# Kernel optimization log

Hardware: AMD Instinct MI355X
Metric: run time of the kernel (lower is better)

Reference implementation:

```python
import jax, jax.numpy as jnp
import numpy as np

BITS = 8
NUM_HEADS = 16
EMB = 1024
MLP = 4096
BATCH = 4
SEQ = 1024


def _fq(x, bits, signed=True, narrow=False):
    """Fake-quantize with per-tensor absmax scale (brevitas MinMax/MaxStats style),
    straight-through-estimator round. signed+narrow => weight quant; signed non-narrow
    => activation quant; unsigned => QuantReLU output."""
    if signed:
        qmax = 2.0 ** (bits - 1) - 1.0
        qmin = -qmax if narrow else -(qmax + 1.0)
    else:
        qmax = 2.0 ** bits - 1.0
        qmin = 0.0
    scale = jax.lax.stop_gradient(jnp.max(jnp.abs(x)) / qmax)
    scale = jnp.maximum(scale, jnp.asarray(1e-8, x.dtype))
    q = x / scale
    q = q + jax.lax.stop_gradient(jnp.round(q) - q)  # STE round
    return jnp.clip(q, qmin, qmax) * scale


def _layernorm(x, eps=1e-5):
    mu = jnp.mean(x, axis=-1, keepdims=True)
    var = jnp.mean(jnp.square(x - mu), axis=-1, keepdims=True)
    return (x - mu) * jax.lax.rsqrt(var + eps)


def setup_inputs() -> dict:
    key = jax.random.key(0)
    ks = jax.random.split(key, 11)
    def w(k, shape, fan_in):
        return jax.random.normal(k, shape, jnp.float32) * (1.0 / np.sqrt(fan_in))
    return {
        "x": jax.random.normal(ks[0], (BATCH, SEQ, EMB), jnp.float32),
        "Wq": w(ks[1], (EMB, EMB), EMB), "bq": jnp.zeros((EMB,), jnp.float32),
        "Wk": w(ks[2], (EMB, EMB), EMB), "bk": jnp.zeros((EMB,), jnp.float32),
        "Wv": w(ks[3], (EMB, EMB), EMB), "bv": jnp.zeros((EMB,), jnp.float32),
        "Wo": w(ks[4], (EMB, EMB), EMB), "bo": jnp.zeros((EMB,), jnp.float32),
        "W1": w(ks[5], (MLP, EMB), EMB), "b1": jnp.zeros((MLP,), jnp.float32),
        "W2": w(ks[6], (EMB, MLP), MLP), "b2": jnp.zeros((EMB,), jnp.float32),
    }


def reference(x, Wq, bq, Wk, bk, Wv, bv, Wo, bo, W1, b1, W2, b2):
    B, S, E = x.shape
    H, D = NUM_HEADS, EMB // NUM_HEADS
    fqw = lambda W: _fq(W, BITS, signed=True, narrow=True)   # weight quant
    fqb = lambda b: _fq(b, BITS, signed=True)                # bias quant
    fqa = lambda a: _fq(a, BITS, signed=True)                # act quant

    # sdp_input_quant
    qx = fqa(x)
    # separate (unpacked) in-projections, torch Linear: y = x @ W.T + b
    q = qx @ fqw(Wq).T + fqb(bq)
    k = qx @ fqw(Wk).T + fqb(bk)
    v = qx @ fqw(Wv).T + fqb(bv)
    # [B,H,S,D]
    q = q.reshape(B, S, H, D).transpose(0, 2, 1, 3)
    k = k.reshape(B, S, H, D).transpose(0, 2, 1, 3)
    v = v.reshape(B, S, H, D).transpose(0, 2, 1, 3)

    q_scaled = fqa(q * (1.0 / np.sqrt(D)))          # q_scaled_quant
    k_t = fqa(k.transpose(0, 1, 3, 2))              # k_transposed_quant
    v = fqa(v)                                      # v_quant

    scores = jnp.einsum('bhqd,bhdk->bhqk', q_scaled, k_t)
    scores = fqa(scores)                            # softmax_input_quant
    attn = jax.nn.softmax(scores, axis=-1)
    attn = fqa(attn)                                # attn_output_weights_quant

    ctx = jnp.einsum('bhqk,bhkd->bhqd', attn, v)
    ctx = ctx.transpose(0, 2, 1, 3).reshape(B, S, E)
    ctx = fqa(ctx)                                  # out_proj_input_quant
    attn_out = ctx @ fqw(Wo).T + fqb(bo)

    # residual_sdp (QuantEltwiseAdd input quant on both operands) + layer-norm
    h = _layernorm(fqa(x) + fqa(attn_out))

    # MLP: QuantIdentity -> QuantLinear -> QuantReLU(unsigned) -> QuantLinear
    m = fqa(h)
    m = m @ fqw(W1).T + fqb(b1)
    m = _fq(jax.nn.relu(m), BITS, signed=False)
    m = m @ fqw(W2).T + fqb(b2)

    return _layernorm(fqa(h) + fqa(m))
```

## Files before the change

kernel.cpp:

```cpp
#include <hip/hip_runtime.h>
#include <cstdint>
#include <cstddef>

#define TB_B 4
#define TB_S 1024
#define TB_E 1024
#define TB_H 16
#define TB_D 64
#define TB_MLP 4096
#define TB_ROWS (TB_B * TB_S)

typedef int int4v __attribute__((ext_vector_type(4)));

#define LGKM0() __asm__ volatile("s_waitcnt lgkmcnt(0)" ::: "memory")
#define CMEMBAR() __asm__ volatile("" ::: "memory")

static __device__ __forceinline__ void atomicMaxF(float* addr, float v) {
  atomicMax(reinterpret_cast<unsigned int*>(addr), __float_as_uint(v));
}

static __device__ __forceinline__ float fast_exp2(float x) {
#if __has_builtin(__builtin_amdgcn_exp2f)
  return __builtin_amdgcn_exp2f(x);
#else
  return exp2f(x);
#endif
}

static __device__ __forceinline__ void gl2lds16(const void* g, void* l) {
  __builtin_amdgcn_global_load_lds(
      (const __attribute__((address_space(1))) void*)g,
      (__attribute__((address_space(3))) void*)l, 16, 0, 0);
}

struct AMDesc { const float* p; long n4; int slot; };
struct AMBatch { AMDesc d[13]; };
__global__ __launch_bounds__(256) void absmax_multi_kernel(AMBatch bt, float* ws) {
  AMDesc d = bt.d[blockIdx.y];
  float m = 0.f;
  long stride = (long)gridDim.x * 256;
  for (long i = (long)blockIdx.x * 256 + threadIdx.x; i < d.n4; i += stride) {
    float4 v = ((const float4*)d.p)[i];
    m = fmaxf(m, fmaxf(fmaxf(fabsf(v.x), fabsf(v.y)), fmaxf(fabsf(v.z), fabsf(v.w))));
  }
#pragma unroll
  for (int o = 32; o; o >>= 1) m = fmaxf(m, __shfl_down(m, o, 64));
  __shared__ float sm[4];
  if (!(threadIdx.x & 63)) sm[threadIdx.x >> 6] = m;
  __syncthreads();
  if (threadIdx.x == 0)
    atomicMaxF(ws + d.slot, fmaxf(fmaxf(sm[0], sm[1]), fmaxf(sm[2], sm[3])));
}

struct QMDesc { const float* in; signed char* out; long n4; int slot; float qmin; };
struct QMBatch { QMDesc d[7]; };
__global__ __launch_bounds__(256) void quant8_multi_kernel(QMBatch bt, const float* ws) {
  QMDesc d = bt.d[blockIdx.y];
  float scale = fmaxf(ws[d.slot] / 127.f, 1e-8f);
  long stride = (long)gridDim.x * 256;
  for (long i = (long)blockIdx.x * 256 + threadIdx.x; i < d.n4; i += stride) {
    float4 v = ((const float4*)d.in)[i];
    char4 o;
    o.x = (signed char)(int)fminf(fmaxf(rintf(v.x / scale), d.qmin), 127.f);
    o.y = (signed char)(int)fminf(fmaxf(rintf(v.y / scale), d.qmin), 127.f);
    o.z = (signed char)(int)fminf(fmaxf(rintf(v.z / scale), d.qmin), 127.f);
    o.w = (signed char)(int)fminf(fmaxf(rintf(v.w / scale), d.qmin), 127.f);
    ((char4*)d.out)[i] = o;
  }
}

struct BDesc { const float* in; float* out; int n4; int slot; };
struct BBatch { BDesc d[6]; };
__global__ __launch_bounds__(256) void bias_quant_multi_kernel(BBatch bt, const float* ws) {
  BDesc d = bt.d[blockIdx.y];
  float scale = fmaxf(ws[d.slot] / 127.f, 1e-8f);
  int i = blockIdx.x * 256 + threadIdx.x;
  if (i < d.n4) {
    float4 v = ((const float4*)d.in)[i];
    float4 o;
    o.x = fminf(fmaxf(rintf(v.x / scale), -128.f), 127.f) * scale;
    o.y = fminf(fmaxf(rintf(v.y / scale), -128.f), 127.f) * scale;
    o.z = fminf(fmaxf(rintf(v.z / scale), -128.f), 127.f) * scale;
    o.w = fminf(fmaxf(rintf(v.w / scale), -128.f), 127.f) * scale;
    ((float4*)d.out)[i] = o;
  }
}

__global__ __launch_bounds__(256) void quant8_kernel(const float* __restrict__ in,
                                                     signed char* __restrict__ out8, long n4,
                                                     const float* __restrict__ amax_p,
                                                     float pre, float qmin) {
  float scale = fmaxf(amax_p[0] * pre / 127.f, 1e-8f);
  long stride = (long)gridDim.x * 256;
  for (long i = (long)blockIdx.x * 256 + threadIdx.x; i < n4; i += stride) {
    float4 v = ((const float4*)in)[i];
    char4 o;
    o.x = (signed char)(int)fminf(fmaxf(rintf(v.x * pre / scale), qmin), 127.f);
    o.y = (signed char)(int)fminf(fmaxf(rintf(v.y * pre / scale), qmin), 127.f);
    o.z = (signed char)(int)fminf(fmaxf(rintf(v.z * pre / scale), qmin), 127.f);
    o.w = (signed char)(int)fminf(fmaxf(rintf(v.w * pre / scale), qmin), 127.f);
    ((char4*)out8)[i] = o;
  }
}

__global__ __launch_bounds__(256) void relu_quant8_kernel(const float* __restrict__ in,
                                                          signed char* __restrict__ out8, long n4,
                                                          const float* __restrict__ amax_p) {
  float scale = fmaxf(amax_p[0] / 255.f, 1e-8f);
  long stride = (long)gridDim.x * 256;
  for (long i = (long)blockIdx.x * 256 + threadIdx.x; i < n4; i += stride) {
    float4 v = ((const float4*)in)[i];
    char4 o;
    o.x = (signed char)((int)fminf(fmaxf(rintf(fmaxf(v.x, 0.f) / scale), 0.f), 255.f) - 128);
    o.y = (signed char)((int)fminf(fmaxf(rintf(fmaxf(v.y, 0.f) / scale), 0.f), 255.f) - 128);
    o.z = (signed char)((int)fminf(fmaxf(rintf(fmaxf(v.z, 0.f) / scale), 0.f), 255.f) - 128);
    o.w = (signed char)((int)fminf(fmaxf(rintf(fmaxf(v.w, 0.f) / scale), 0.f), 255.f) - 128);
    ((char4*)out8)[i] = o;
  }
}

__global__ __launch_bounds__(256) void rowsum_i8_kernel(const signed char* __restrict__ w8,
                                                        int* __restrict__ out, int Kdim) {
  const int row = blockIdx.x, t = threadIdx.x;
  const signed char* p = w8 + (long)row * Kdim;
  int s = 0;
  for (int i = t * 16; i < Kdim; i += 4096) {
    int4v v = *(const int4v*)(p + i);
    const signed char* b = (const signed char*)&v;
#pragma unroll
    for (int j = 0; j < 16; j++) s += b[j];
  }
#pragma unroll
  for (int o = 32; o; o >>= 1) s += __shfl_down(s, o, 64);
  __shared__ int sm[4];
  if (!(t & 63)) sm[t >> 6] = s;
  __syncthreads();
  if (t == 0) out[row] = sm[0] + sm[1] + sm[2] + sm[3];
}

__global__ __launch_bounds__(256) void gemm_i8_kernel(
    const signed char* __restrict__ A, const signed char* __restrict__ Bw,
    const float* __restrict__ biasq,
    const float* __restrict__ amax_a, float div_a,
    const float* __restrict__ amax_b,
    const int* __restrict__ rowsum,
    float* __restrict__ C, int M, int N, int K,
    float* __restrict__ amax_out, int relu_amax, int mode) {
  __shared__ signed char As[8192];
  __shared__ signed char Bs[8192];
  const int t = threadIdx.x;
  int bx, by;
  {
    int lin = blockIdx.y * gridDim.x + blockIdx.x;
    if ((gridDim.y & 7) == 0) {
      int xcd = lin & 7, j = lin >> 3;
      bx = j % gridDim.x;
      by = (gridDim.y >> 3) * xcd + j / gridDim.x;
    } else { bx = blockIdx.x; by = blockIdx.y; }
  }
  const int m0 = by * 128, n0 = bx * 128;
  const int w = t >> 6, lane = t & 63;
  const int fr = lane & 15, quad = lane >> 4;
  const int r0 = t >> 2;
  const int c0 = (t & 3) * 16;
  const int a_off0 = (w * 32 + fr) * 64 + quad * 16;
  const int b_off0 = fr * 64 + quad * 16;

  int4v acc[2][8];
#pragma unroll
  for (int r = 0; r < 2; r++)
#pragma unroll
    for (int c = 0; c < 8; c++) acc[r][c] = (int4v){0, 0, 0, 0};

  for (int k0 = 0; k0 < K; k0 += 64) {
    __syncthreads();
    gl2lds16(A + (long)(m0 + r0) * K + k0 + c0, As + t * 16);
    gl2lds16(A + (long)(m0 + r0 + 64) * K + k0 + c0, As + t * 16 + 4096);
    gl2lds16(Bw + (long)(n0 + r0) * K + k0 + c0, Bs + t * 16);
    gl2lds16(Bw + (long)(n0 + r0 + 64) * K + k0 + c0, Bs + t * 16 + 4096);
    __syncthreads();
    int4v af[2], bf[8];
#pragma unroll
    for (int r = 0; r < 2; r++) af[r] = *(const int4v*)(As + a_off0 + r * 1024);
#pragma unroll
    for (int c = 0; c < 8; c++) bf[c] = *(const int4v*)(Bs + b_off0 + c * 1024);
#pragma unroll
    for (int r = 0; r < 2; r++)
#pragma unroll
      for (int c = 0; c < 8; c++)
        acc[r][c] = __builtin_amdgcn_mfma_i32_16x16x64_i8(af[r], bf[c], acc[r][c], 0, 0, 0);
  }

  const int seg = (mode == 1) ? (n0 >> 10) : 0;
  const float s_a = fmaxf(amax_a[0] / div_a, 1e-8f);
  const float s_b = fmaxf(amax_b[seg] / 127.f, 1e-8f);
  const float s = s_a * s_b;
  float lmax = 0.f;
#pragma unroll
  for (int r = 0; r < 2; r++) {
    int rbase = m0 + w * 32 + r * 16 + quad * 4;
#pragma unroll
    for (int c = 0; c < 8; c++) {
      int col = n0 + c * 16 + fr;
      int corr = rowsum ? (rowsum[col] << 7) : 0;
      float bi = biasq[col];
      if (mode == 1) {
        int h = (col >> 6) & 15, dd = col & 63;
        float* cbase = C + (long)seg * ((long)TB_ROWS * TB_E);
#pragma unroll
        for (int g = 0; g < 4; g++) {
          int m = rbase + g;
          int b = m >> 10, sdx = m & 1023;
          float o = (float)acc[r][c][g] * s + bi;
          lmax = fmaxf(lmax, fabsf(o));
          cbase[((((long)b * TB_H + h) * TB_S) + sdx) * TB_D + dd] = o;
        }
      } else {
#pragma unroll
        for (int g = 0; g < 4; g++) {
          float o = (float)(acc[r][c][g] + corr) * s + bi;
          lmax = fmaxf(lmax, relu_amax ? fmaxf(o, 0.f) : fabsf(o));
          C[(long)(rbase + g) * N + col] = o;
        }
      }
    }
  }
#pragma unroll
  for (int o = 32; o; o >>= 1) lmax = fmaxf(lmax, __shfl_down(lmax, o, 64));
  __shared__ float redm[4];
  if (!lane) redm[w] = lmax;
  __syncthreads();
  if (t == 0) atomicMaxF(amax_out + seg, fmaxf(fmaxf(redm[0], redm[1]), fmaxf(redm[2], redm[3])));
}

__global__ __launch_bounds__(256) void quant8_vb_kernel(const float* __restrict__ v,
                                                        const float* __restrict__ amax_p,
                                                        signed char* __restrict__ v8b) {
  __shared__ signed char tile[64][80];
  const int bh = blockIdx.x;
  const int jb = blockIdx.y;
  const int s0 = jb * 64;
  const int t = threadIdx.x;
  const float scale = fmaxf(amax_p[0] / 127.f, 1e-8f);
#pragma unroll
  for (int it = 0; it < 4; it++) {
    int idx = t + it * 256;
    int r = idx >> 4, c4 = (idx & 15) * 4;
    float4 vv = *(const float4*)(v + ((long)bh * TB_S + s0 + r) * TB_D + c4);
    tile[c4 + 0][r] = (signed char)(int)fminf(fmaxf(rintf(vv.x / scale), -128.f), 127.f);
    tile[c4 + 1][r] = (signed char)(int)fminf(fmaxf(rintf(vv.y / scale), -128.f), 127.f);
    tile[c4 + 2][r] = (signed char)(int)fminf(fmaxf(rintf(vv.z / scale), -128.f), 127.f);
    tile[c4 + 3][r] = (signed char)(int)fminf(fmaxf(rintf(vv.w / scale), -128.f), 127.f);
  }
  __syncthreads();
  int d = t >> 2, sb = (t & 3) * 16;
  int4v o = *(const int4v*)&tile[d][sb];
  *(int4v*)(v8b + (((long)bh * 16 + jb) * 64 + d) * 64 + sb) = o;
}

__global__ __launch_bounds__(256) void attn_rowmax_kernel(const signed char* __restrict__ q8,
                                                          const signed char* __restrict__ k8,
                                                          int* __restrict__ irowmax,
                                                          int* __restrict__ imax_out) {
  const int bh = blockIdx.x;
  const int t = threadIdx.x, w = t >> 6, lane = t & 63;
  const int fr = lane & 15, quad = lane >> 4;
  const int i0 = blockIdx.y * 64 + w * 16;
  const long base = (long)bh * TB_S;
  int4v qf = *(const int4v*)(q8 + (base + i0 + fr) * 64 + quad * 16);
  int mx = -2147483647, mn = 2147483647;
  for (int j0 = 0; j0 < TB_S; j0 += 16) {
    int4v kf = *(const int4v*)(k8 + (base + j0 + fr) * 64 + quad * 16);
    int4v sc = __builtin_amdgcn_mfma_i32_16x16x64_i8(kf, qf, (int4v){0, 0, 0, 0}, 0, 0, 0);
    mx = max(mx, max(max(sc[0], sc[1]), max(sc[2], sc[3])));
    mn = min(mn, min(min(sc[0], sc[1]), min(sc[2], sc[3])));
  }
  mx = max(mx, __shfl_xor(mx, 16, 64));
  mx = max(mx, __shfl_xor(mx, 32, 64));
  mn = min(mn, __shfl_xor(mn, 16, 64));
  mn = min(mn, __shfl_xor(mn, 32, 64));
  if (quad == 0) irowmax[(long)bh * TB_S + i0 + fr] = mx;
  int gm = max(mx, -mn);
#pragma unroll
  for (int o = 32; o; o >>= 1) gm = max(gm, __shfl_down(gm, o, 64));
  __shared__ int sm[4];
  if (!lane) sm[w] = gm;
  __syncthreads();
  if (t == 0) atomicMax(imax_out, max(max(sm[0], sm[1]), max(sm[2], sm[3])));
}

__global__ __launch_bounds__(256) void attn_rowsum_kernel(
    const signed char* __restrict__ q8, const signed char* __restrict__ k8,
    const int* __restrict__ irowmax, const int* __restrict__ imax_p,
    const float* __restrict__ amax_q, const float* __restrict__ amax_k,
    float* __restrict__ rowl, float* __restrict__ amax_attn) {
  const int bh = blockIdx.x;
  const int t = threadIdx.x, w = t >> 6, lane = t & 63;
  const int fr = lane & 15, quad = lane >> 4;
  const int i0 = blockIdx.y * 64 + w * 16;
  const float s_q = fmaxf(amax_q[0] * 0.125f / 127.f, 1e-8f);
  const float s_k = fmaxf(amax_k[0] / 127.f, 1e-8f);
  const float sqk = s_q * s_k;
  const float s_sc = fmaxf((float)imax_p[0] * sqk / 127.f, 1e-8f);
  const float c1 = sqk / s_sc;
  const float aa = s_sc * 1.44269504088896340736f;
  const long base = (long)bh * TB_S;
  int4v qf = *(const int4v*)(q8 + (base + i0 + fr) * 64 + quad * 16);
  const int imr = irowmax[base + i0 + fr];
  const float qmax = fminf(fmaxf(rintf((float)imr * c1), -128.f), 127.f);
  const float qa = qmax * aa;
  float l = 0.f;
  for (int j0 = 0; j0 < TB_S; j0 += 16) {
    int4v kf = *(const int4v*)(k8 + (base + j0 + fr) * 64 + quad * 16);
    int4v sc = __builtin_amdgcn_mfma_i32_16x16x64_i8(kf, qf, (int4v){0, 0, 0, 0}, 0, 0, 0);
#pragma unroll
    for (int g = 0; g < 4; g++) {
      float qv = fminf(fmaxf(rintf((float)sc[g] * c1), -128.f), 127.f);
      l += fast_exp2(fmaf(qv, aa, -qa));
    }
  }
  l += __shfl_xor(l, 16, 64);
  l += __shfl_xor(l, 32, 64);
  if (quad == 0) rowl[base + i0 + fr] = l;
  float inv = 1.f / l;
#pragma unroll
  for (int o = 32; o; o >>= 1) inv = fmaxf(inv, __shfl_down(inv, o, 64));
  __shared__ float smf[4];
  if (!lane) smf[w] = inv;
  __syncthreads();
  if (t == 0) atomicMaxF(amax_attn, fmaxf(fmaxf(smf[0], smf[1]), fmaxf(smf[2], smf[3])));
}

__global__ __launch_bounds__(256) void attn_pv_kernel(
    const signed char* __restrict__ q8, const signed char* __restrict__ k8,
    const signed char* __restrict__ v8b,
    const int* __restrict__ irowmax, const int* __restrict__ imax_p,
    const float* __restrict__ amax_q, const float* __restrict__ amax_k,
    const float* __restrict__ amax_v, const float* __restrict__ amax_attn,
    const float* __restrict__ rowl,
    float* __restrict__ ctx, float* __restrict__ amax_ctx) {
  __shared__ signed char latt[4][16][80];
  const int bh = blockIdx.x, b = bh >> 4, h = bh & 15;
  const int t = threadIdx.x, w = t >> 6, lane = t & 63;
  const int fr = lane & 15, quad = lane >> 4;
  const int i0 = blockIdx.y * 64 + w * 16;
  const float s_q = fmaxf(amax_q[0] * 0.125f / 127.f, 1e-8f);
  const float s_k = fmaxf(amax_k[0] / 127.f, 1e-8f);
  const float sqk = s_q * s_k;
  const float s_sc = fmaxf((float)imax_p[0] * sqk / 127.f, 1e-8f);
  const float c1 = sqk / s_sc;
  const float aa = s_sc * 1.44269504088896340736f;
  const float s_v = fmaxf(amax_v[0] / 127.f, 1e-8f);
  const float s_at = fmaxf(amax_attn[0] / 127.f, 1e-8f);
  const long base = (long)bh * TB_S;
  int4v qf = *(const int4v*)(q8 + (base + i0 + fr) * 64 + quad * 16);
  const int imr = irowmax[base + i0 + fr];
  const float qmax = fminf(fmaxf(rintf((float)imr * c1), -128.f), 127.f);
  const float bexp = qmax * aa;
  const float li = rowl[base + i0 + fr];
  const float invls = 1.f / (li * s_at);
  int4v accv[4];
#pragma unroll
  for (int dtile = 0; dtile < 4; dtile++) accv[dtile] = (int4v){0, 0, 0, 0};

  for (int j0 = 0; j0 < TB_S; j0 += 64) {
#pragma unroll
    for (int tt = 0; tt < 4; tt++) {
      int4v kf = *(const int4v*)(k8 + (base + j0 + tt * 16 + fr) * 64 + quad * 16);
      int4v sc = __builtin_amdgcn_mfma_i32_16x16x64_i8(kf, qf, (int4v){0, 0, 0, 0}, 0, 0, 0);
      int packed = 0;
#pragma unroll
      for (int g = 0; g < 4; g++) {
        float qv = fminf(fmaxf(rintf((float)sc[g] * c1), -128.f), 127.f);
        float e = fast_exp2(fmaf(qv, aa, -bexp));
        int code = (int)fminf(fmaxf(rintf(e * invls), -128.f), 127.f);
        packed |= (code & 255) << (g * 8);
      }
      *(int*)&latt[w][fr][tt * 16 + quad * 4] = packed;
    }
    LGKM0();
    int4v af = *(const int4v*)&latt[w][fr][quad * 16];
    const signed char* vbase = v8b + (((long)bh * 16 + (j0 >> 6)) * 64) * 64;
#pragma unroll
    for (int dtile = 0; dtile < 4; dtile++) {
      int4v vf = *(const int4v*)(vbase + (dtile * 16 + fr) * 64 + quad * 16);
      accv[dtile] = __builtin_amdgcn_mfma_i32_16x16x64_i8(af, vf, accv[dtile], 0, 0, 0);
    }
    CMEMBAR();
  }
  const float sav = s_at * s_v;
  float cmax = 0.f;
#pragma unroll
  for (int dtile = 0; dtile < 4; dtile++) {
#pragma unroll
    for (int g = 0; g < 4; g++) {
      float val = (float)accv[dtile][g] * sav;
      cmax = fmaxf(cmax, fabsf(val));
      int irow = i0 + quad * 4 + g;
      ctx[(((long)(b * TB_S + irow)) * TB_H + h) * TB_D + dtile * 16 + fr] = val;
    }
  }
#pragma unroll
  for (int o = 32; o; o >>= 1) cmax = fmaxf(cmax, __shfl_down(cmax, o, 64));
  __shared__ float smf[4];
  if (!lane) smf[w] = cmax;
  __syncthreads();
  if (t == 0) atomicMaxF(amax_ctx, fmaxf(fmaxf(smf[0], smf[1]), fmaxf(smf[2], smf[3])));
}

__global__ __launch_bounds__(256) void resid_ln_kernel(const signed char* __restrict__ a8,
                                                       const float* __restrict__ amax_a,
                                                       const float* __restrict__ braw,
                                                       const float* __restrict__ amax_b,
                                                       float* __restrict__ outp,
                                                       float* __restrict__ amax_out) {
  __shared__ float red[4];
  __shared__ float redm[4];
  const int row = blockIdx.x, t = threadIdx.x;
  const float sa = fmaxf(amax_a[0] / 127.f, 1e-8f);
  const float sb = fmaxf(amax_b[0] / 127.f, 1e-8f);
  const long base = (long)row * TB_E + t * 4;
  char4 a = ((const char4*)a8)[(long)row * 256 + t];
  float4 bv = *(const float4*)(braw + base);
  float v0 = (float)a.x * sa + fminf(fmaxf(rintf(bv.x / sb), -128.f), 127.f) * sb;
  float v1 = (float)a.y * sa + fminf(fmaxf(rintf(bv.y / sb), -128.f), 127.f) * sb;
  float v2 = (float)a.z * sa + fminf(fmaxf(rintf(bv.z / sb), -128.f), 127.f) * sb;
  float v3 = (float)a.w * sa + fminf(fmaxf(rintf(bv.w / sb), -128.f), 127.f) * sb;
  float s = v0 + v1 + v2 + v3;
#pragma unroll
  for (int o = 32; o; o >>= 1) s += __shfl_down(s, o, 64);
  if (!(t & 63)) red[t >> 6] = s;
  __syncthreads();
  float mu = ((red[0] + red[1]) + (red[2] + red[3])) * (1.f / TB_E);
  float d0 = v0 - mu, d1 = v1 - mu, d2 = v2 - mu, d3 = v3 - mu;
  float sq = d0 * d0 + d1 * d1 + d2 * d2 + d3 * d3;
#pragma unroll
  for (int o = 32; o; o >>= 1) sq += __shfl_down(sq, o, 64);
  __syncthreads();
  if (!(t & 63)) red[t >> 6] = sq;
  __syncthreads();
  float var = ((red[0] + red[1]) + (red[2] + red[3])) * (1.f / TB_E);
  float rs = 1.f / sqrtf(var + 1e-5f);
  float4 o4;
  o4.x = d0 * rs; o4.y = d1 * rs; o4.z = d2 * rs; o4.w = d3 * rs;
  *(float4*)(outp + base) = o4;
  float lm = fmaxf(fmaxf(fabsf(o4.x), fabsf(o4.y)), fmaxf(fabsf(o4.z), fabsf(o4.w)));
#pragma unroll
  for (int o = 32; o; o >>= 1) lm = fmaxf(lm, __shfl_down(lm, o, 64));
  if (!(t & 63)) redm[t >> 6] = lm;
  __syncthreads();
  if (t == 0) atomicMaxF(amax_out, fmaxf(fmaxf(redm[0], redm[1]), fmaxf(redm[2], redm[3])));
}

#define SL_X 0
#define SL_WQ 1
#define SL_WK 2
#define SL_WV 3
#define SL_WO 4
#define SL_W1 5
#define SL_W2 6
#define SL_BQ 7
#define SL_BK 8
#define SL_BV 9
#define SL_BO 10
#define SL_B1 11
#define SL_B2 12
#define SL_Q 13
#define SL_K 14
#define SL_V 15
#define SL_SCI 16
#define SL_ATTN 17
#define SL_CTX 18
#define SL_AO 19
#define SL_H 20
#define SL_RELU 21
#define SL_M2 22
#define SL_DUMMY 23

static inline int nblocks(long n) {
  long b = (n + 255) / 256;
  return (int)(b > 2048 ? 2048 : b);
}

extern "C" void kernel_launch(void* const* d_in, const int* in_sizes, int n_in,
                              void* d_out, int out_size, void* d_ws, size_t ws_size,
                              hipStream_t stream) {
  const float* x  = (const float*)d_in[0];
  const float* Wq = (const float*)d_in[1];
  const float* bq = (const float*)d_in[2];
  const float* Wk = (const float*)d_in[3];
  const float* bk = (const float*)d_in[4];
  const float* Wv = (const float*)d_in[5];
  const float* bv = (const float*)d_in[6];
  const float* Wo = (const float*)d_in[7];
  const float* bo = (const float*)d_in[8];
  const float* W1 = (const float*)d_in[9];
  const float* b1 = (const float*)d_in[10];
  const float* W2 = (const float*)d_in[11];
  const float* b2 = (const float*)d_in[12];
  float* ws = (float*)d_ws;
  float* out = (float*)d_out;

  const long SZ_XE = (long)TB_ROWS * TB_E;
  const long SZ_W  = (long)TB_E * TB_E;
  const long SZ_M1 = (long)TB_ROWS * TB_MLP;

  const long OFF_QBQ = 1024, OFF_QBK = 2048, OFF_QBV = 3072, OFF_QBO = 4096;
  const long OFF_QB1 = 5120, OFF_QB2 = 9216;
  const long OFF_RSUM = 10240;
  const long OFF_Q  = 65536;
  const long OFF_K  = OFF_Q + SZ_XE;
  const long OFF_V  = OFF_K + SZ_XE;
  const long OFF_M2 = OFF_V + SZ_XE;
  const long OFF_IRM = OFF_M2 + SZ_XE;
  const long OFF_ROWL = OFF_IRM + 65536;
  const long OFF_M1 = OFF_ROWL + 65536;
  const long OFF_I8 = OFF_M1 + SZ_M1;

  float* qbuf = ws + OFF_Q;  float* kbuf = ws + OFF_K;  float* vbuf = ws + OFF_V;
  float* m2   = ws + OFF_M2;
  int*   irowmax = (int*)(ws + OFF_IRM);
  float* rowl = ws + OFF_ROWL;
  float* m1 = ws + OFF_M1;
  float* ctx = qbuf;
  float* attn_out = kbuf;
  float* hbuf = vbuf;
  float* qbq_ = ws + OFF_QBQ; float* qbk_ = ws + OFF_QBK;
  float* qbv_ = ws + OFF_QBV; float* qbo_ = ws + OFF_QBO;
  float* qb1_ = ws + OFF_QB1; float* qb2_ = ws + OFF_QB2;
  int* rsum = (int*)(ws + OFF_RSUM);
  int* imax = (int*)(ws + SL_SCI);

  signed char* i8base = (signed char*)(ws + OFF_I8);
  signed char* qx8  = i8base;
  signed char* wq8  = qx8 + SZ_XE;
  signed char* wk8  = wq8 + SZ_W;
  signed char* wv8  = wk8 + SZ_W;
  signed char* wo8  = wv8 + SZ_W;
  signed char* w18  = wo8 + SZ_W;
  signed char* w28  = w18 + SZ_XE;
  signed char* ctx8 = w28 + SZ_XE;
  signed char* m08  = ctx8 + SZ_XE;
  signed char* m18  = m08 + SZ_XE;
  signed char* q8   = m18 + SZ_M1;
  signed char* k8   = q8 + SZ_XE;
  signed char* v8b  = k8 + SZ_XE;

  hipMemsetAsync(ws, 0, 4096, stream);

  AMBatch am;
  am.d[0]  = {x,  SZ_XE/4, SL_X};
  am.d[1]  = {Wq, SZ_W/4,  SL_WQ};
  am.d[2]  = {Wk, SZ_W/4,  SL_WK};
  am.d[3]  = {Wv, SZ_W/4,  SL_WV};
  am.d[4]  = {Wo, SZ_W/4,  SL_WO};
  am.d[5]  = {W1, SZ_XE/4, SL_W1};
  am.d[6]  = {W2, SZ_XE/4, SL_W2};
  am.d[7]  = {bq, 256,     SL_BQ};
  am.d[8]  = {bk, 256,     SL_BK};
  am.d[9]  = {bv, 256,     SL_BV};
  am.d[10] = {bo, 256,     SL_BO};
  am.d[11] = {b1, 1024,    SL_B1};
  am.d[12] = {b2, 256,     SL_B2};
  absmax_multi_kernel<<<dim3(64, 13), 256, 0, stream>>>(am, ws);

  QMBatch qm;
  qm.d[0] = {x,  qx8, SZ_XE/4, SL_X,  -128.f};
  qm.d[1] = {Wq, wq8, SZ_W/4,  SL_WQ, -127.f};
  qm.d[2] = {Wk, wk8, SZ_W/4,  SL_WK, -127.f};
  qm.d[3] = {Wv, wv8, SZ_W/4,  SL_WV, -127.f};
  qm.d[4] = {W1, w18, SZ_XE/4, SL_W1, -127.f};
  qm.d[5] = {W2, w28, SZ_XE/4, SL_W2, -127.f};
  qm.d[6] = {Wo, wo8, SZ_W/4,  SL_WO, -127.f};
  quant8_multi_kernel<<<dim3(64, 7), 256, 0, stream>>>(qm, ws);
  rowsum_i8_kernel<<<TB_E, 256, 0, stream>>>(w28, rsum, TB_MLP);
  BBatch bb;
  bb.d[0] = {bq, qbq_, 256,  SL_BQ};
  bb.d[1] = {bk, qbk_, 256,  SL_BK};
  bb.d[2] = {bv, qbv_, 256,  SL_BV};
  bb.d[3] = {bo, qbo_, 256,  SL_BO};
  bb.d[4] = {b1, qb1_, 1024, SL_B1};
  bb.d[5] = {b2, qb2_, 256,  SL_B2};
  bias_quant_multi_kernel<<<dim3(4, 6), 256, 0, stream>>>(bb, ws);

  gemm_i8_kernel<<<dim3(3*TB_E/128, TB_ROWS/128), 256, 0, stream>>>(
      qx8, wq8, qbq_, ws + SL_X, 127.f, ws + SL_WQ, nullptr, qbuf,
      TB_ROWS, 3*TB_E, TB_E, ws + SL_Q, 0, 1);

  quant8_kernel<<<2048, 256, 0, stream>>>(qbuf, q8, SZ_XE/4, ws + SL_Q, 0.125f, -128.f);
  quant8_kernel<<<2048, 256, 0, stream>>>(kbuf, k8, SZ_XE/4, ws + SL_K, 1.f, -128.f);
  quant8_vb_kernel<<<dim3(TB_B*TB_H, TB_S/64), 256, 0, stream>>>(vbuf, ws + SL_V, v8b);

  attn_rowmax_kernel<<<dim3(TB_B*TB_H, TB_S/64), 256, 0, stream>>>(q8, k8, irowmax, imax);
  attn_rowsum_kernel<<<dim3(TB_B*TB_H, TB_S/64), 256, 0, stream>>>(
      q8, k8, irowmax, imax, ws + SL_Q, ws + SL_K, rowl, ws + SL_ATTN);
  attn_pv_kernel<<<dim3(TB_B*TB_H, TB_S/64), 256, 0, stream>>>(
      q8, k8, v8b, irowmax, imax, ws + SL_Q, ws + SL_K, ws + SL_V, ws + SL_ATTN,
      rowl, ctx, ws + SL_CTX);

  quant8_kernel<<<2048, 256, 0, stream>>>(ctx, ctx8, SZ_XE/4, ws + SL_CTX, 1.f, -128.f);
  gemm_i8_kernel<<<dim3(TB_E/128, TB_ROWS/128), 256, 0, stream>>>(
      ctx8, wo8, qbo_, ws + SL_CTX, 127.f, ws + SL_WO, nullptr, attn_out,
      TB_ROWS, TB_E, TB_E, ws + SL_AO, 0, 0);

  resid_ln_kernel<<<TB_ROWS, 256, 0, stream>>>(qx8, ws + SL_X, attn_out, ws + SL_AO, hbuf, ws + SL_H);

  quant8_kernel<<<2048, 256, 0, stream>>>(hbuf, m08, SZ_XE/4, ws + SL_H, 1.f, -128.f);
  gemm_i8_kernel<<<dim3(TB_MLP/128, TB_ROWS/128), 256, 0, stream>>>(
      m08, w18, qb1_, ws + SL_H, 127.f, ws + SL_W1, nullptr, m1,
      TB_ROWS, TB_MLP, TB_E, ws + SL_RELU, 1, 0);
  relu_quant8_kernel<<<nblocks(SZ_M1/4), 256, 0, stream>>>(m1, m18, SZ_M1/4, ws + SL_RELU);
  gemm_i8_kernel<<<dim3(TB_E/128, TB_ROWS/128), 256, 0, stream>>>(
      m18, w28, qb2_, ws + SL_RELU, 255.f, ws + SL_W2, rsum, m2,
      TB_ROWS, TB_E, TB_MLP, ws + SL_M2, 0, 0);

  resid_ln_kernel<<<TB_ROWS, 256, 0, stream>>>(m08, ws + SL_H, m2, ws + SL_M2, out, ws + SL_DUMMY);
}
```

Measured before the change: 556.0 us.

## Double-buffer int8 GEMM LDS tiles, swizzle layout, use 2x2 warp tiling

The int8 GEMM kernel now keeps two LDS buffers per operand and issues the global-to-LDS load of the next K-tile before computing on the current one, so memory latency overlaps with MFMA work. The LDS layout gets an XOR swizzle on the 16-byte column chunk to cut bank conflicts on fragment reads. Each wave's tile changes from 32x128 to 64x64 (2x2 wave grid), which lowers total fragment loads per MFMA. In exchange, LDS use doubles, which may reduce occupancy, and the loop assumes the K-tile count is even.

```diff
diff --git a/kernel.cpp b/kernel.cpp
--- a/kernel.cpp
+++ b/kernel.cpp
@@ -146,8 +146,8 @@
     const int* __restrict__ rowsum,
     float* __restrict__ C, int M, int N, int K,
     float* __restrict__ amax_out, int relu_amax, int mode) {
-  __shared__ signed char As[8192];
-  __shared__ signed char Bs[8192];
+  __shared__ signed char As[2][8192];
+  __shared__ signed char Bs[2][8192];
   const int t = threadIdx.x;
   int bx, by;
   {
@@ -161,34 +161,53 @@
   const int m0 = by * 128, n0 = bx * 128;
   const int w = t >> 6, lane = t & 63;
   const int fr = lane & 15, quad = lane >> 4;
+  const int wm = w >> 1, wn = w & 1;
   const int r0 = t >> 2;
-  const int c0 = (t & 3) * 16;
-  const int a_off0 = (w * 32 + fr) * 64 + quad * 16;
-  const int b_off0 = fr * 64 + quad * 16;
-
-  int4v acc[2][8];
-#pragma unroll
-  for (int r = 0; r < 2; r++)
-#pragma unroll
-    for (int c = 0; c < 8; c++) acc[r][c] = (int4v){0, 0, 0, 0};
-
-  for (int k0 = 0; k0 < K; k0 += 64) {
+  const int csrc = (((t & 3) ^ ((t >> 3) & 3)) << 4);
+  const int sx = ((quad ^ ((fr >> 1) & 3)) << 4);
+
+  int4v acc[4][4];
+#pragma unroll
+  for (int r = 0; r < 4; r++)
+#pragma unroll
+    for (int c = 0; c < 4; c++) acc[r][c] = (int4v){0, 0, 0, 0};
+
+  const long arow0 = (long)(m0 + r0) * K + csrc;
+  const long arow1 = (long)(m0 + r0 + 64) * K + csrc;
+  const long brow0 = (long)(n0 + r0) * K + csrc;
+  const long brow1 = (long)(n0 + r0 + 64) * K + csrc;
+
+  auto stage = [&](int buf, int kk) {
+    gl2lds16(A + arow0 + kk, As[buf] + t * 16);
+    gl2lds16(A + arow1 + kk, As[buf] + t * 16 + 4096);
+    gl2lds16(Bw + brow0 + kk, Bs[buf] + t * 16);
+    gl2lds16(Bw + brow1 + kk, Bs[buf] + t * 16 + 4096);
+  };
+  auto compute = [&](int buf) {
+    int4v af[4], bf[4];
+#pragma unroll
+    for (int r = 0; r < 4; r++)
+      af[r] = *(const int4v*)(As[buf] + (wm * 64 + r * 16 + fr) * 64 + sx);
+#pragma unroll
+    for (int c = 0; c < 4; c++)
+      bf[c] = *(const int4v*)(Bs[buf] + (wn * 64 + c * 16 + fr) * 64 + sx);
+#pragma unroll
+    for (int r = 0; r < 4; r++)
+#pragma unroll
+      for (int c = 0; c < 4; c++)
+        acc[r][c] = __builtin_amdgcn_mfma_i32_16x16x64_i8(af[r], bf[c], acc[r][c], 0, 0, 0);
+  };
+
+  const int nt = K >> 6;
+  stage(0, 0);
+  __syncthreads();
+  for (int kt = 0; kt < nt; kt += 2) {
+    stage(1, (kt + 1) << 6);
+    compute(0);
     __syncthreads();
-    gl2lds16(A + (long)(m0 + r0) * K + k0 + c0, As + t * 16);
-    gl2lds16(A + (long)(m0 + r0 + 64) * K + k0 + c0, As + t * 16 + 4096);
-    gl2lds16(Bw + (long)(n0 + r0) * K + k0 + c0, Bs + t * 16);
-    gl2lds16(Bw + (long)(n0 + r0 + 64) * K + k0 + c0, Bs + t * 16 + 4096);
+    if (kt + 2 < nt) stage(0, (kt + 2) << 6);
+    compute(1);
     __syncthreads();
-    int4v af[2], bf[8];
-#pragma unroll
-    for (int r = 0; r < 2; r++) af[r] = *(const int4v*)(As + a_off0 + r * 1024);
-#pragma unroll
-    for (int c = 0; c < 8; c++) bf[c] = *(const int4v*)(Bs + b_off0 + c * 1024);
-#pragma unroll
-    for (int r = 0; r < 2; r++)
-#pragma unroll
-      for (int c = 0; c < 8; c++)
-        acc[r][c] = __builtin_amdgcn_mfma_i32_16x16x64_i8(af[r], bf[c], acc[r][c], 0, 0, 0);
   }
 
   const int seg = (mode == 1) ? (n0 >> 10) : 0;
@@ -197,11 +216,11 @@
   const float s = s_a * s_b;
   float lmax = 0.f;
 #pragma unroll
-  for (int r = 0; r < 2; r++) {
-    int rbase = m0 + w * 32 + r * 16 + quad * 4;
-#pragma unroll
-    for (int c = 0; c < 8; c++) {
-      int col = n0 + c * 16 + fr;
+  for (int r = 0; r < 4; r++) {
+    int rbase = m0 + wm * 64 + r * 16 + quad * 4;
+#pragma unroll
+    for (int c = 0; c < 4; c++) {
+      int col = n0 + wn * 64 + c * 16 + fr;
       int corr = rowsum ? (rowsum[col] << 7) : 0;
       float bi = biasq[col];
       if (mode == 1) {
```

Measured after the change: 551.3 us. About the same (-0.9%).
